# Performance work log

Hardware: AMD Instinct MI355X
Metric: run time of the kernel (lower is better)

Reference implementation:

```python
import jax, jax.numpy as jnp
import numpy as np

DIM = 256
CTX_DIM = 768
GROUPS = 8
EPS = 1e-5


def setup_inputs() -> dict:
    key = jax.random.key(0)
    ks = jax.random.split(key, 16)
    B, C, H, W, L = 16, DIM, 64, 64, 77
    s_conv = 1.0 / np.sqrt(C * 9)
    s_q = 1.0 / np.sqrt(C)
    s_kv = 1.0 / np.sqrt(CTX_DIM)
    return {
        "x": jax.random.normal(ks[0], (B, C, H, W), jnp.float32),
        "context": jax.random.normal(ks[1], (B, L, CTX_DIM), jnp.float32),
        "conv_w": jax.random.uniform(ks[2], (C, C, 3, 3), jnp.float32, -s_conv, s_conv),
        "conv_b": jax.random.uniform(ks[3], (C,), jnp.float32, -s_conv, s_conv),
        "gn_w": jnp.ones((C,), jnp.float32),
        "gn_b": jnp.zeros((C,), jnp.float32),
        "wq": jax.random.uniform(ks[4], (C, C), jnp.float32, -s_q, s_q),
        "bq": jax.random.uniform(ks[5], (C,), jnp.float32, -s_q, s_q),
        "wk": jax.random.uniform(ks[6], (C, CTX_DIM), jnp.float32, -s_kv, s_kv),
        "bk": jax.random.uniform(ks[7], (C,), jnp.float32, -s_kv, s_kv),
        "wv": jax.random.uniform(ks[8], (C, CTX_DIM), jnp.float32, -s_kv, s_kv),
        "bv": jax.random.uniform(ks[9], (C,), jnp.float32, -s_kv, s_kv),
        "wo": jax.random.uniform(ks[10], (C, C), jnp.float32, -s_q, s_q),
        "bo": jax.random.uniform(ks[11], (C,), jnp.float32, -s_q, s_q),
    }


def _group_norm(h, gn_w, gn_b):
    B, C, H, W = h.shape
    g = h.reshape(B, GROUPS, C // GROUPS, H, W)
    mean = g.mean(axis=(2, 3, 4), keepdims=True)
    var = g.var(axis=(2, 3, 4), keepdims=True)
    g = (g - mean) * jax.lax.rsqrt(var + EPS)
    h = g.reshape(B, C, H, W)
    return h * gn_w[None, :, None, None] + gn_b[None, :, None, None]


def reference(x, context, conv_w, conv_b, gn_w, gn_b, wq, bq, wk, bk, wv, bv, wo, bo):
    B, C, H, W = x.shape
    # conv 3x3, padding=1 (NCHW, OIHW)
    h = jax.lax.conv_general_dilated(
        x, conv_w, window_strides=(1, 1), padding=((1, 1), (1, 1)),
        dimension_numbers=("NCHW", "OIHW", "NCHW"))
    h = h + conv_b[None, :, None, None]
    h = jax.nn.silu(_group_norm(h, gn_w, gn_b))
    # flatten spatial -> tokens: [B, HW, C]
    hf = h.reshape(B, C, H * W).transpose(0, 2, 1)
    q = hf @ wq.T + bq                     # [B, HW, C]
    k = context @ wk.T + bk                # [B, L, C]
    v = context @ wv.T + bv                # [B, L, C]
    scale = 1.0 / jnp.sqrt(jnp.asarray(C, q.dtype))
    att = jax.nn.softmax(jnp.einsum("bqc,bkc->bqk", q, k) * scale, axis=-1)
    o = jnp.einsum("bqk,bkc->bqc", att, v) @ wo.T + bo
    h_att = o.transpose(0, 2, 1).reshape(B, C, H, W)
    return x + h_att
```

## Files before the change

### kernel.cpp

```cpp
#include <hip/hip_runtime.h>
#include <stdint.h>

#define B_  16
#define C_  256
#define HW_ 4096
#define Hp  66
#define PP  4356
#define EPS_ 1e-5f

typedef unsigned short u16;
typedef unsigned int   u32;
typedef __attribute__((ext_vector_type(4))) float  f32x4;
typedef __attribute__((ext_vector_type(8))) __bf16 bf16x8;
typedef __attribute__((ext_vector_type(8))) u16    u16x8;

__device__ __forceinline__ float bf2f(u16 u){ u32 x = ((u32)u)<<16; float f; __builtin_memcpy(&f,&x,4); return f; }
__device__ __forceinline__ u16 f2bf(float f){ u32 x; __builtin_memcpy(&x,&f,4); u32 r = x + 0x7fffu + ((x>>16)&1u); return (u16)(r>>16); }

__device__ __forceinline__ void g2l16(const void* g, void* l){
  __builtin_amdgcn_global_load_lds((__attribute__((address_space(1))) void*)(void*)g,
                                   (__attribute__((address_space(3))) void*)l, 16, 0, 0);
}
__device__ __forceinline__ bf16x8 ldfrag(const u16* p){
  u16x8 r = *(const u16x8*)p;
  return __builtin_bit_cast(bf16x8, r);
}

__global__ __launch_bounds__(256) void k_prep(const float* __restrict__ x, u16* __restrict__ xpT,
    const float* __restrict__ conv_w, const float* __restrict__ wq, const float* __restrict__ wo,
    const float* __restrict__ wk, const float* __restrict__ wv, const float* __restrict__ ctx,
    u16* __restrict__ wBt, u16* __restrict__ wqB, u16* __restrict__ woB,
    u16* __restrict__ wkvB, u16* __restrict__ ctxB, float* __restrict__ stats){
  __shared__ float Lt[64*65];
  int bid = blockIdx.x; int tid = threadIdx.x;
  if(bid >= 1056){
    int i = (bid-1056)*256 + tid;
    if(i < 589824){
      int j = i&7, co = (i>>3)&255, atom = (i>>11)&3, g = i>>13;
      int t = g%9, cic = g/9;
      int ciF = cic*32 + atom*8 + j;
      wBt[i] = f2bf(conv_w[(co*256+ciF)*9 + t]); return;
    }
    i -= 589824;
    if(i < 65536){ wqB[i] = f2bf(wq[i]); return; } i -= 65536;
    if(i < 65536){ woB[i] = f2bf(wo[i]); return; } i -= 65536;
    if(i < 196608){ wkvB[i] = f2bf(wk[i]); return; } i -= 196608;
    if(i < 196608){ wkvB[196608+i] = f2bf(wv[i]); return; } i -= 196608;
    if(i < 946176){ ctxB[i] = f2bf(ctx[i]); return; } i -= 946176;
    if(i < 512){ stats[i] = 0.f; }
    return;
  }
  int b = bid/66, hh = bid - b*66;
  if(hh==0 || hh==65){
    for(int i=tid;i<32*264;i+=256){
      int pl = i/264, off = i - pl*264;
      u32* p = (u32*)(xpT + ((size_t)(b*32+pl)*PP + (size_t)hh*Hp)*8);
      p[off] = 0u;
    }
    return;
  }
  {
    int pl = tid>>3, q = tid&7;
    size_t base = ((size_t)(b*32+pl)*PP + (size_t)hh*Hp + (q>=4?65:0))*8;
    ((u32*)(xpT + base))[q&3] = 0u;
  }
  int h = hh-1;
  for(int cc=0; cc<4; cc++){
    int c0=cc*64;
    int ci = tid>>2, w0 = (tid&3)*16;
    const float* xs = x + ((size_t)(b*C_ + c0+ci)*HW_) + h*64 + w0;
    for(int j=0;j<4;j++){
      float4 v = *(const float4*)(xs + j*4);
      Lt[ci*65 + w0 + j*4 + 0] = v.x;
      Lt[ci*65 + w0 + j*4 + 1] = v.y;
      Lt[ci*65 + w0 + j*4 + 2] = v.z;
      Lt[ci*65 + w0 + j*4 + 3] = v.w;
    }
    __syncthreads();
    int w = tid>>2, cj = (tid&3)*16;
    union { u16 u[16]; uint4 v[2]; } outu;
    for(int j=0;j<16;j++) outu.u[j] = f2bf(Lt[(cj+j)*65 + w]);
    int chan = c0 + cj;
    int cic = chan>>5, at0 = (chan>>3)&3;
    u16* dst = xpT + (((size_t)(b*8+cic)*4 + at0)*PP + (size_t)hh*Hp + w + 1)*8;
    *(uint4*)dst = outu.v[0];
    *(uint4*)(dst + (size_t)PP*8) = outu.v[1];
    __syncthreads();
  }
}

__global__ __launch_bounds__(256, 3) void k_conv(const u16* __restrict__ xpT, const u16* __restrict__ wBt,
    const float* __restrict__ conv_b, u16* __restrict__ h, float* __restrict__ stats){
  __shared__ u16 As[2][264*32];
  __shared__ u16 Bs[2][128*32];
  int bid0 = blockIdx.x;
  int l = (bid0 & 7)*128 + (bid0 >> 3);
  int b = l >> 6, hp = (l >> 1) & 31, nh = l & 1;
  int tid = threadIdx.x;
  int w = tid>>6, lane = tid&63, ln = lane&15, qd = lane>>4;
  int wm = w&1, wn = w>>1;
  f32x4 acc[4][4] = {};
  int hr_[4], wp_[4];
  #pragma unroll
  for(int mf=0;mf<4;mf++){ int p = wm*64 + mf*16 + ln; hr_[mf] = p>>6; wp_[mf] = p&63; }

  #pragma unroll
  for(int r=0;r<5;r++){
    int c = r*256 + tid;
    if(c < 1056){
      int atom = c/264, ipix = c - atom*264;
      g2l16(xpT + (((size_t)(b*8+0)*4 + atom)*PP + hp*132 + ipix)*8, &As[0][c*8]);
    }
  }
  #pragma unroll
  for(int r=0;r<2;r++){
    int c = r*256 + tid;
    int atom = c>>7, col = c&127;
    g2l16(wBt + ((size_t)atom*2048 + (nh*128+col)*8), &Bs[0][c*8]);
  }
  __syncthreads();

  int cb = 0;
  for(int ci=0; ci<8; ci++){
    int ca = ci&1;
    for(int t=0;t<9;t++){
      int tn = t+1, cin = ci;
      if(tn==9){ tn=0; cin=ci+1; }
      if(cin < 8){
        #pragma unroll
        for(int r=0;r<2;r++){
          int c = r*256 + tid;
          int atom = c>>7, col = c&127;
          g2l16(wBt + (((size_t)(cin*9+tn)*4 + atom)*2048 + (nh*128+col)*8), &Bs[cb^1][c*8]);
        }
      }
      if(t<5 && ci<7){
        int c = t*256 + tid;
        if(c < 1056){
          int atom = c/264, ipix = c - atom*264;
          g2l16(xpT + (((size_t)(b*8+ci+1)*4 + atom)*PP + hp*132 + ipix)*8, &As[ca^1][c*8]);
        }
      }
      int dy = (t*11)>>5, dx = t - dy*3;
      bf16x8 af[4], bfv[4];
      #pragma unroll
      for(int mf=0;mf<4;mf++){
        int ipix = (hr_[mf]+dy)*66 + wp_[mf] + dx;
        af[mf] = ldfrag(&As[ca][(qd*264 + ipix)*8]);
      }
      #pragma unroll
      for(int nf=0;nf<4;nf++) bfv[nf] = ldfrag(&Bs[cb][(qd*128 + wn*64+nf*16+ln)*8]);
      #pragma unroll
      for(int mf=0;mf<4;mf++)
        #pragma unroll
        for(int nf=0;nf<4;nf++)
          acc[mf][nf] = __builtin_amdgcn_mfma_f32_16x16x32_bf16(af[mf], bfv[nf], acc[mf][nf], 0,0,0);
      __syncthreads();
      cb ^= 1;
    }
  }
  float s[2]={0,0}, q[2]={0,0};
  int p0 = hp*128;
  for(int nf=0;nf<4;nf++){
    int n = nh*128 + wn*64 + nf*16 + ln;
    float bias = conv_b[n];
    for(int mf=0;mf<4;mf++){
      for(int r=0;r<4;r++){
        int p = wm*64 + mf*16 + qd*4 + r;
        float v = acc[mf][nf][r] + bias;
        h[((size_t)(b*HW_ + p0 + p))*C_ + n] = f2bf(v);
        s[nf>>1]+=v; q[nf>>1]+=v*v;
      }
    }
  }
  for(int off=32;off>=1;off>>=1){
    #pragma unroll
    for(int g=0;g<2;g++){ s[g]+=__shfl_down(s[g],off,64); q[g]+=__shfl_down(q[g],off,64); }
  }
  if(lane==0){
    #pragma unroll
    for(int g=0;g<2;g++){
      int gg = nh*4 + wn*2 + g;
      atomicAdd(&stats[(b*8 + gg)*2+0], s[g]);
      atomicAdd(&stats[(b*8 + gg)*2+1], q[g]);
    }
  }
}

__global__ __launch_bounds__(256, 2) void k_qgn(const u16* __restrict__ hbuf, const u16* __restrict__ wqB,
    const float* __restrict__ stats, const float* __restrict__ gnw, const float* __restrict__ gnb,
    const float* __restrict__ bq, u16* __restrict__ qb){
  __shared__ u16 As[128*32];
  __shared__ u16 Bs[256*32];
  int mt = blockIdx.x;
  int b = mt >> 5;
  int tid = threadIdx.x;
  int w = tid>>6, lane = tid&63, ln = lane&15, qd = lane>>4;
  int wm = w&1, wn = w>>1;
  int pr = tid>>1, half = tid&1;
  const u16* hsrc = hbuf + ((size_t)(mt*128+pr))*256 + half*16;
  f32x4 acc[4][8] = {};
  uint4 ra0, ra1, rb0, rb1;
  ra0 = *(const uint4*)(hsrc);
  ra1 = *(const uint4*)(hsrc + 8);
  for(int kt=0; kt<8; kt++){
    float sm = stats[(b*8+kt)*2], qm = stats[(b*8+kt)*2+1];
    float mean = sm*(1.f/131072.f);
    float rstd = rsqrtf(qm*(1.f/131072.f) - mean*mean + EPS_);
    int c0 = kt*32 + half*16;
    float4 gw0 = *(const float4*)(gnw+c0), gw1 = *(const float4*)(gnw+c0+4);
    float4 gw2 = *(const float4*)(gnw+c0+8), gw3 = *(const float4*)(gnw+c0+12);
    float4 gb0 = *(const float4*)(gnb+c0), gb1 = *(const float4*)(gnb+c0+4);
    float4 gb2 = *(const float4*)(gnb+c0+8), gb3 = *(const float4*)(gnb+c0+12);
    float gwv[16] = {gw0.x,gw0.y,gw0.z,gw0.w, gw1.x,gw1.y,gw1.z,gw1.w,
                     gw2.x,gw2.y,gw2.z,gw2.w, gw3.x,gw3.y,gw3.z,gw3.w};
    float gbv[16] = {gb0.x,gb0.y,gb0.z,gb0.w, gb1.x,gb1.y,gb1.z,gb1.w,
                     gb2.x,gb2.y,gb2.z,gb2.w, gb3.x,gb3.y,gb3.z,gb3.w};
    u16 inu[16];
    ((uint4*)inu)[0] = ra0; ((uint4*)inu)[1] = ra1;
    u16 outu[16];
    #pragma unroll
    for(int j=0;j<16;j++){
      float v = bf2f(inu[j]);
      v = (v-mean)*rstd*gwv[j] + gbv[j];
      float s = v/(1.f+__expf(-v));
      outu[j] = f2bf(s);
    }
    u16* adst = &As[pr*32 + half*16];
    ((uint4*)adst)[0] = ((uint4*)outu)[0];
    ((uint4*)adst)[1] = ((uint4*)outu)[1];
    #pragma unroll
    for(int r=0;r<4;r++){
      int c = r*256 + tid;
      int co = c>>2, atom = c&3;
      g2l16(wqB + (size_t)co*256 + kt*32 + atom*8, &Bs[c*8]);
    }
    if(kt<7){
      rb0 = *(const uint4*)(hsrc + (kt+1)*32);
      rb1 = *(const uint4*)(hsrc + (kt+1)*32 + 8);
    }
    __syncthreads();
    bf16x8 af[4], bfv[8];
    #pragma unroll
    for(int mf=0;mf<4;mf++) af[mf] = ldfrag(&As[(wm*64+mf*16+ln)*32 + qd*8]);
    #pragma unroll
    for(int nf=0;nf<8;nf++) bfv[nf] = ldfrag(&Bs[(wn*128+nf*16+ln)*32 + qd*8]);
    #pragma unroll
    for(int mf=0;mf<4;mf++)
      #pragma unroll
      for(int nf=0;nf<8;nf++)
        acc[mf][nf] = __builtin_amdgcn_mfma_f32_16x16x32_bf16(af[mf], bfv[nf], acc[mf][nf], 0,0,0);
    __syncthreads();
    ra0 = rb0; ra1 = rb1;
  }
  for(int nf=0;nf<8;nf++){
    int n = wn*128 + nf*16 + ln;
    float bias = bq[n];
    for(int mf=0;mf<4;mf++){
      for(int r=0;r<4;r++){
        int ml = wm*64 + mf*16 + qd*4 + r;
        qb[((size_t)(mt*128+ml))*256 + n] = f2bf(acc[mf][nf][r]+bias);
      }
    }
  }
}

__global__ __launch_bounds__(256) void k_kvproj(const u16* __restrict__ ctxB, const u16* __restrict__ wkvB,
    const float* __restrict__ bk, const float* __restrict__ bv,
    u16* __restrict__ kb, u16* __restrict__ vT){
  __shared__ u16 As[64*128];
  __shared__ u16 Bs[64*128];
  int bid = blockIdx.x;
  int nt = bid & 7, mt = bid >> 3;
  int n0 = nt*64, m0 = mt*64;
  int tid=threadIdx.x, w=tid>>6, lane=tid&63, ln=lane&15, qd=lane>>4;
  int wm = w&1, wn = w>>1;
  f32x4 acc[2][2]={};
  for(int kt=0;kt<6;kt++){
    #pragma unroll
    for(int r=0;r<4;r++){
      int c = r*256 + tid;
      int row = c>>4, atom = c&15;
      g2l16(ctxB + ((size_t)(m0+row)*768 + kt*128 + atom*8), &As[c*8]);
      g2l16(wkvB + ((size_t)(n0+row)*768 + kt*128 + atom*8), &Bs[c*8]);
    }
    __syncthreads();
    #pragma unroll
    for(int kk=0;kk<4;kk++){
      bf16x8 af[2], bfv[2];
      #pragma unroll
      for(int mf=0;mf<2;mf++) af[mf]=ldfrag(&As[(wm*32+mf*16+ln)*128 + kk*32 + qd*8]);
      #pragma unroll
      for(int nf=0;nf<2;nf++) bfv[nf]=ldfrag(&Bs[(wn*32+nf*16+ln)*128 + kk*32 + qd*8]);
      #pragma unroll
      for(int mf=0;mf<2;mf++)
        #pragma unroll
        for(int nf=0;nf<2;nf++)
          acc[mf][nf]=__builtin_amdgcn_mfma_f32_16x16x32_bf16(af[mf],bfv[nf],acc[mf][nf],0,0,0);
    }
    __syncthreads();
  }
  for(int mf=0;mf<2;mf++) for(int nf=0;nf<2;nf++){
    int ng = n0 + wn*32 + nf*16 + ln;
    float bias = ng<256 ? bk[ng] : bv[ng-256];
    for(int r=0;r<4;r++){
      int mg = m0 + wm*32 + mf*16 + qd*4 + r;
      if(mg<1232){
        float v=acc[mf][nf][r]+bias;
        int bb=mg/77, l=mg-bb*77;
        if(ng<256) kb[((size_t)(bb*77+l))*256+ng]=f2bf(v);
        else vT[((size_t)(bb*256+(ng-256)))*96 + l]=f2bf(v);
      }
    }
  }
}

__global__ __launch_bounds__(256, 2) void k_attn(const u16* __restrict__ qg, const u16* __restrict__ kb,
    const u16* __restrict__ vT, u16* __restrict__ ob){
  __shared__ u16 KVf[3072*8];
  __shared__ u16 Pb[128*104];
  __shared__ float invr[128];
  int bid=blockIdx.x; int b=bid>>5, qt=bid&31; int p0=qt*128;
  int tid=threadIdx.x, w=tid>>6, lane=tid&63, ln=lane&15, qd=lane>>4;

  #pragma unroll
  for(int j=0;j<10;j++){
    int c = tid + j*256;
    int kt = c/320, rem = c - kt*320;
    int q2 = rem/80, l = rem - q2*80;
    int ls = l<77 ? l : 76;
    g2l16(kb + ((size_t)(b*77+ls)*256 + kt*32 + q2*8), &KVf[(size_t)c*8]);
  }
  bf16x8 qf[2][8];
  #pragma unroll
  for(int mf=0;mf<2;mf++){
    const u16* qsrc = qg + ((size_t)(b*HW_ + p0 + w*32 + mf*16 + ln))*256 + qd*8;
    #pragma unroll
    for(int kt=0;kt<8;kt++) qf[mf][kt] = ldfrag(qsrc + kt*32);
  }
  __syncthreads();

  f32x4 Sa[2][5]={};
  #pragma unroll
  for(int kt=0;kt<8;kt++){
    bf16x8 kf[5];
    #pragma unroll
    for(int nf=0;nf<5;nf++) kf[nf]=ldfrag(&KVf[((size_t)kt*320 + qd*80 + nf*16+ln)*8]);
    #pragma unroll
    for(int mf=0;mf<2;mf++)
      #pragma unroll
      for(int nf=0;nf<5;nf++)
        Sa[mf][nf]=__builtin_amdgcn_mfma_f32_16x16x32_bf16(qf[mf][kt],kf[nf],Sa[mf][nf],0,0,0);
  }
  if(ln>=13){
    #pragma unroll
    for(int mf=0;mf<2;mf++)
      #pragma unroll
      for(int r=0;r<4;r++) Sa[mf][4][r] = -1e30f;
  }
  float mrow[2][4];
  #pragma unroll
  for(int mf=0;mf<2;mf++)
    #pragma unroll
    for(int r=0;r<4;r++){
      float m = Sa[mf][0][r];
      #pragma unroll
      for(int nf=1;nf<5;nf++) m = fmaxf(m, Sa[mf][nf][r]);
      mrow[mf][r]=m;
    }
  #pragma unroll
  for(int off=1;off<16;off<<=1)
    #pragma unroll
    for(int mf=0;mf<2;mf++)
      #pragma unroll
      for(int r=0;r<4;r++) mrow[mf][r] = fmaxf(mrow[mf][r], __shfl_xor(mrow[mf][r], off, 64));
  float rs[2][4]={};
  u16 pe[2][5][4];
  #pragma unroll
  for(int mf=0;mf<2;mf++)
    #pragma unroll
    for(int nf=0;nf<5;nf++)
      #pragma unroll
      for(int r=0;r<4;r++){
        float e = __expf((Sa[mf][nf][r]-mrow[mf][r])*0.0625f);
        rs[mf][r]+=e; pe[mf][nf][r]=f2bf(e);
      }
  #pragma unroll
  for(int off=1;off<16;off<<=1)
    #pragma unroll
    for(int mf=0;mf<2;mf++)
      #pragma unroll
      for(int r=0;r<4;r++) rs[mf][r] += __shfl_xor(rs[mf][r], off, 64);
  #pragma unroll
  for(int mf=0;mf<2;mf++)
    #pragma unroll
    for(int nf=0;nf<5;nf++)
      #pragma unroll
      for(int r=0;r<4;r++) Pb[(w*32+mf*16+qd*4+r)*104 + nf*16+ln] = pe[mf][nf][r];
  {
    int row = tid>>1, j0 = (tid&1)*8;
    u16x8 z = {0,0,0,0,0,0,0,0};
    *(u16x8*)&Pb[row*104 + 80 + j0] = z;
  }
  if(ln==0){
    #pragma unroll
    for(int mf=0;mf<2;mf++)
      #pragma unroll
      for(int r=0;r<4;r++) invr[w*32+mf*16+qd*4+r] = 1.f/rs[mf][r];
  }
  __syncthreads();

  #pragma unroll
  for(int j=0;j<12;j++){
    int c = tid + j*256;
    int g = c>>7, co = c&127;
    int q2 = g&3, s5 = g>>2;
    int nh2 = s5>2 ? 1 : 0, kt2 = s5 - 3*nh2;
    g2l16(vT + ((size_t)(b*256 + nh2*128 + co)*96 + kt2*32 + q2*8), &KVf[(size_t)c*8]);
  }
  __syncthreads();

  #pragma unroll
  for(int nh=0;nh<2;nh++){
    f32x4 Oa[2][8]={};
    #pragma unroll
    for(int kt2=0;kt2<3;kt2++){
      bf16x8 pa[2], vf[8];
      #pragma unroll
      for(int mf=0;mf<2;mf++) pa[mf]=ldfrag(&Pb[(w*32+mf*16+ln)*104 + kt2*32+qd*8]);
      #pragma unroll
      for(int nf=0;nf<8;nf++) vf[nf]=ldfrag(&KVf[(((size_t)(nh*3+kt2)*4+qd)*128 + nf*16+ln)*8]);
      #pragma unroll
      for(int mf=0;mf<2;mf++)
        #pragma unroll
        for(int nf=0;nf<8;nf++)
          Oa[mf][nf]=__builtin_amdgcn_mfma_f32_16x16x32_bf16(pa[mf],vf[nf],Oa[mf][nf],0,0,0);
    }
    #pragma unroll
    for(int mf=0;mf<2;mf++){
      #pragma unroll
      for(int r=0;r<4;r++){
        int ml=w*32+mf*16+qd*4+r;
        float inv = invr[ml];
        #pragma unroll
        for(int nf=0;nf<8;nf++){
          int nl=nh*128+nf*16+ln;
          ob[((size_t)(b*HW_+p0+ml))*256+nl]=f2bf(Oa[mf][nf][r]*inv);
        }
      }
    }
  }
}

__global__ __launch_bounds__(256) void k_oproj(const u16* __restrict__ ob, const u16* __restrict__ woB,
    const float* __restrict__ bo, const float* __restrict__ x, float* __restrict__ outp){
  __shared__ u16 As[128*32];
  __shared__ u16 Bs[128*32];
  int bid=blockIdx.x;
  int b=bid>>6; int rr=bid&63; int cm=rr>>5, pt=rr&31;
  int c0=cm*128, p0=pt*128;
  int tid=threadIdx.x, w=tid>>6, lane=tid&63, ln=lane&15, qd=lane>>4, wm=w>>1, wn=w&1;
  int srow=tid>>2, koff=(tid&3)*8;
  f32x4 acc[4][4]={};
  for(int kt=0;kt<8;kt++){
    for(int j=0;j<2;j++){
      int m=srow+j*64;
      g2l16(woB + ((size_t)(c0+m)*256 + kt*32+koff),        &As[(size_t)tid*8+j*2048]);
      g2l16(ob  + ((size_t)(b*HW_+p0+m)*256 + kt*32+koff),  &Bs[(size_t)tid*8+j*2048]);
    }
    __syncthreads();
    bf16x8 af[4], bfv[4];
    for(int mf=0;mf<4;mf++) af[mf]=ldfrag(&As[(wm*64+mf*16+ln)*32+qd*8]);
    for(int nf=0;nf<4;nf++) bfv[nf]=ldfrag(&Bs[(wn*64+nf*16+ln)*32+qd*8]);
    for(int mf=0;mf<4;mf++) for(int nf=0;nf<4;nf++)
      acc[mf][nf]=__builtin_amdgcn_mfma_f32_16x16x32_bf16(af[mf],bfv[nf],acc[mf][nf],0,0,0);
    __syncthreads();
  }
  for(int mf=0;mf<4;mf++) for(int r=0;r<4;r++){
    int cl=c0+wm*64+mf*16+qd*4+r;
    float bias=bo[cl];
    for(int nf=0;nf<4;nf++){
      int pl=p0+wn*64+nf*16+ln;
      size_t idx=((size_t)(b*C_+cl))*HW_+pl;
      outp[idx]=x[idx]+acc[mf][nf][r]+bias;
    }
  }
}

extern "C" void kernel_launch(void* const* d_in, const int* in_sizes, int n_in,
                              void* d_out, int out_size, void* d_ws, size_t ws_size,
                              hipStream_t stream){
  const float* x      = (const float*)d_in[0];
  const float* ctx    = (const float*)d_in[1];
  const float* conv_w = (const float*)d_in[2];
  const float* conv_b = (const float*)d_in[3];
  const float* gnw    = (const float*)d_in[4];
  const float* gnb    = (const float*)d_in[5];
  const float* wq     = (const float*)d_in[6];
  const float* bq     = (const float*)d_in[7];
  const float* wk     = (const float*)d_in[8];
  const float* bk     = (const float*)d_in[9];
  const float* wv     = (const float*)d_in[10];
  const float* bv     = (const float*)d_in[11];
  const float* wo     = (const float*)d_in[12];
  const float* bo     = (const float*)d_in[13];
  char* ws = (char*)d_ws;
  u16* xpT  = (u16*)(ws + 0);
  u16* wBt  = (u16*)(ws + 35684352);
  u16* wqB  = (u16*)(ws + 36864000);
  u16* wkvB = (u16*)(ws + 36995072);
  u16* woB  = (u16*)(ws + 37781504);
  u16* ctxB = (u16*)(ws + 37912576);
  u16* hbuf = (u16*)(ws + 39804928);
  u16* kbv  = (u16*)(ws + 73359360);
  u16* vT   = (u16*)(ws + 73990144);
  u16* obuf = (u16*)(ws + 74776576);
  float* stats = (float*)(ws + 108331008);
  u16* qb = xpT;
  float* outp = (float*)d_out;

  k_prep  <<<9106, 256, 0, stream>>>(x, xpT, conv_w, wq, wo, wk, wv, ctx, wBt, wqB, woB, wkvB, ctxB, stats);
  k_conv  <<<1024, 256, 0, stream>>>(xpT, wBt, conv_b, hbuf, stats);
  k_qgn   <<<512,  256, 0, stream>>>(hbuf, wqB, stats, gnw, gnb, bq, qb);
  k_kvproj<<<160,  256, 0, stream>>>(ctxB, wkvB, bk, bv, kbv, vT);
  k_attn  <<<512,  256, 0, stream>>>(qb, kbv, vT, obuf);
  k_oproj <<<1024, 256, 0, stream>>>(obuf, woB, bo, x, outp);
}
```

Before: 366.3 us.

## Fuse output projection and residual add into attention kernel

The attention kernel now keeps its normalized output tile in shared memory and runs the Wo projection directly from there, adding bias and the residual x before writing the final result. This drops the separate k_oproj launch and the bf16 round trip of the attention output through global memory. In exchange, accumulator registers grow (Oa for both halves plus a 4x8 projection accumulator) under a two-blocks-per-CU launch bound, so spilling or lower occupancy is a risk. Wo fragments are also read straight from global memory by every block instead of being staged in LDS.

Measured after the change: 338.8 us. 1.08x faster.

```diff
diff --git a/kernel.cpp b/kernel.cpp
--- a/kernel.cpp
+++ b/kernel.cpp
@@ -316,10 +316,13 @@
 }
 
 __global__ __launch_bounds__(256, 2) void k_attn(const u16* __restrict__ qg, const u16* __restrict__ kb,
-    const u16* __restrict__ vT, u16* __restrict__ ob){
-  __shared__ u16 KVf[3072*8];
-  __shared__ u16 Pb[128*104];
+    const u16* __restrict__ vT, const u16* __restrict__ woB, const float* __restrict__ bo,
+    const float* __restrict__ x, float* __restrict__ outp){
+  __shared__ u16 SM[37888];
   __shared__ float invr[128];
+  u16* KVf = SM;
+  u16* Pb  = SM + 24576;
+  u16* Ol  = SM;
   int bid=blockIdx.x; int b=bid>>5, qt=bid&31; int p0=qt*128;
   int tid=threadIdx.x, w=tid>>6, lane=tid&63, ln=lane&15, qd=lane>>4;
 
@@ -420,9 +423,9 @@
   }
   __syncthreads();
 
+  f32x4 Oa[2][2][8]={};
   #pragma unroll
   for(int nh=0;nh<2;nh++){
-    f32x4 Oa[2][8]={};
     #pragma unroll
     for(int kt2=0;kt2<3;kt2++){
       bf16x8 pa[2], vf[8];
@@ -434,57 +437,54 @@
       for(int mf=0;mf<2;mf++)
         #pragma unroll
         for(int nf=0;nf<8;nf++)
-          Oa[mf][nf]=__builtin_amdgcn_mfma_f32_16x16x32_bf16(pa[mf],vf[nf],Oa[mf][nf],0,0,0);
-    }
-    #pragma unroll
-    for(int mf=0;mf<2;mf++){
+          Oa[nh][mf][nf]=__builtin_amdgcn_mfma_f32_16x16x32_bf16(pa[mf],vf[nf],Oa[nh][mf][nf],0,0,0);
+    }
+  }
+  __syncthreads();
+
+  #pragma unroll
+  for(int nh=0;nh<2;nh++)
+    #pragma unroll
+    for(int mf=0;mf<2;mf++)
       #pragma unroll
       for(int r=0;r<4;r++){
-        int ml=w*32+mf*16+qd*4+r;
+        int ml = w*32+mf*16+qd*4+r;
         float inv = invr[ml];
         #pragma unroll
-        for(int nf=0;nf<8;nf++){
-          int nl=nh*128+nf*16+ln;
-          ob[((size_t)(b*HW_+p0+ml))*256+nl]=f2bf(Oa[mf][nf][r]*inv);
-        }
-      }
-    }
-  }
-}
-
-__global__ __launch_bounds__(256) void k_oproj(const u16* __restrict__ ob, const u16* __restrict__ woB,
-    const float* __restrict__ bo, const float* __restrict__ x, float* __restrict__ outp){
-  __shared__ u16 As[128*32];
-  __shared__ u16 Bs[128*32];
-  int bid=blockIdx.x;
-  int b=bid>>6; int rr=bid&63; int cm=rr>>5, pt=rr&31;
-  int c0=cm*128, p0=pt*128;
-  int tid=threadIdx.x, w=tid>>6, lane=tid&63, ln=lane&15, qd=lane>>4, wm=w>>1, wn=w&1;
-  int srow=tid>>2, koff=(tid&3)*8;
-  f32x4 acc[4][4]={};
+        for(int nf=0;nf<8;nf++)
+          Ol[ml*264 + nh*128 + nf*16 + ln] = f2bf(Oa[nh][mf][nf][r]*inv);
+      }
+  __syncthreads();
+
+  f32x4 a2[4][8] = {};
+  #pragma unroll 2
   for(int kt=0;kt<8;kt++){
-    for(int j=0;j<2;j++){
-      int m=srow+j*64;
-      g2l16(woB + ((size_t)(c0+m)*256 + kt*32+koff),        &As[(size_t)tid*8+j*2048]);
-      g2l16(ob  + ((size_t)(b*HW_+p0+m)*256 + kt*32+koff),  &Bs[(size_t)tid*8+j*2048]);
-    }
-    __syncthreads();
-    bf16x8 af[4], bfv[4];
-    for(int mf=0;mf<4;mf++) af[mf]=ldfrag(&As[(wm*64+mf*16+ln)*32+qd*8]);
-    for(int nf=0;nf<4;nf++) bfv[nf]=ldfrag(&Bs[(wn*64+nf*16+ln)*32+qd*8]);
-    for(int mf=0;mf<4;mf++) for(int nf=0;nf<4;nf++)
-      acc[mf][nf]=__builtin_amdgcn_mfma_f32_16x16x32_bf16(af[mf],bfv[nf],acc[mf][nf],0,0,0);
-    __syncthreads();
-  }
-  for(int mf=0;mf<4;mf++) for(int r=0;r<4;r++){
-    int cl=c0+wm*64+mf*16+qd*4+r;
-    float bias=bo[cl];
-    for(int nf=0;nf<4;nf++){
-      int pl=p0+wn*64+nf*16+ln;
-      size_t idx=((size_t)(b*C_+cl))*HW_+pl;
-      outp[idx]=x[idx]+acc[mf][nf][r]+bias;
-    }
-  }
+    bf16x8 af2[4], bf2v[8];
+    #pragma unroll
+    for(int mf2=0;mf2<4;mf2++)
+      af2[mf2] = ldfrag(woB + (size_t)(w*64+mf2*16+ln)*256 + kt*32 + qd*8);
+    #pragma unroll
+    for(int nf2=0;nf2<8;nf2++)
+      bf2v[nf2] = ldfrag(&Ol[(nf2*16+ln)*264 + kt*32 + qd*8]);
+    #pragma unroll
+    for(int mf2=0;mf2<4;mf2++)
+      #pragma unroll
+      for(int nf2=0;nf2<8;nf2++)
+        a2[mf2][nf2] = __builtin_amdgcn_mfma_f32_16x16x32_bf16(af2[mf2], bf2v[nf2], a2[mf2][nf2],0,0,0);
+  }
+  #pragma unroll
+  for(int mf2=0;mf2<4;mf2++)
+    #pragma unroll
+    for(int r=0;r<4;r++){
+      int cl = w*64 + mf2*16 + qd*4 + r;
+      float bias = bo[cl];
+      #pragma unroll
+      for(int nf2=0;nf2<8;nf2++){
+        int px = p0 + nf2*16 + ln;
+        size_t idx = ((size_t)(b*C_+cl))*HW_ + px;
+        outp[idx] = x[idx] + a2[mf2][nf2][r] + bias;
+      }
+    }
 }
 
 extern "C" void kernel_launch(void* const* d_in, const int* in_sizes, int n_in,
@@ -514,7 +514,6 @@
   u16* hbuf = (u16*)(ws + 39804928);
   u16* kbv  = (u16*)(ws + 73359360);
   u16* vT   = (u16*)(ws + 73990144);
-  u16* obuf = (u16*)(ws + 74776576);
   float* stats = (float*)(ws + 108331008);
   u16* qb = xpT;
   float* outp = (float*)d_out;
@@ -523,6 +522,5 @@
   k_conv  <<<1024, 256, 0, stream>>>(xpT, wBt, conv_b, hbuf, stats);
   k_qgn   <<<512,  256, 0, stream>>>(hbuf, wqB, stats, gnw, gnb, bq, qb);
   k_kvproj<<<160,  256, 0, stream>>>(ctxB, wkvB, bk, bv, kbv, vT);
-  k_attn  <<<512,  256, 0, stream>>>(qb, kbv, vT, obuf);
-  k_oproj <<<1024, 256, 0, stream>>>(obuf, woB, bo, x, outp);
-}
+  k_attn  <<<512,  256, 0, stream>>>(qb, kbv, vT, woB, bo, x, outp);
+}
```
